# Kernel optimization log

Measured on AMD Instinct MI355X. Metric: run time of the kernel, lower is better.

## Reference

```python
import jax, jax.numpy as jnp
import numpy as np
from jax import lax

K = 3           # number of channel clusters (hard-coded in the torch forward)
KM_ITERS = 50   # fixed Lloyd iterations (stand-in for sklearn KMeans, random_state=0)

SEQ_LEN, PRED_LEN, CH, BATCH = 1024, 192, 1000, 32
LH = SEQ_LEN // 2


def _pairwise_sqdist(z, c):
    # z: [N, D], c: [K, D] -> [N, K]
    zz = jnp.sum(z * z, axis=1, keepdims=True)          # [N,1]
    cc = jnp.sum(c * c, axis=1)[None, :]                # [1,K]
    return zz - 2.0 * (z @ c.T) + cc


def kmeans_labels(z, k=K, iters=KM_ITERS):
    # Deterministic Lloyd's algorithm; init = first k rows (deterministic stand-in
    # for sklearn's k-means++ with random_state=0).
    c0 = z[:k]

    def step(c, _):
        d = _pairwise_sqdist(z, c)
        labels = jnp.argmin(d, axis=1)
        ones = jnp.ones((z.shape[0],), z.dtype)
        sums = jax.ops.segment_sum(z, labels, num_segments=k)       # [K,D]
        counts = jax.ops.segment_sum(ones, labels, num_segments=k)  # [K]
        new_c = jnp.where(counts[:, None] > 0,
                          sums / jnp.maximum(counts, 1.0)[:, None], c)
        return new_c, None

    c, _ = lax.scan(step, c0, None, length=iters)
    return jnp.argmin(_pairwise_sqdist(z, c), axis=1)   # [N] int32


def setup_inputs() -> dict:
    key = jax.random.key(0)
    ks = jax.random.split(key, 4)
    x = jax.random.normal(ks[0], (BATCH, SEQ_LEN, CH), dtype=jnp.float32)
    # stacked per-cluster expert Linears g1/g2/g3: weight [K, P, Lh], bias [K, P]
    Wg = jax.random.normal(ks[1], (K, PRED_LEN, LH), dtype=jnp.float32) * 0.02
    bg = jnp.zeros((K, PRED_LEN), dtype=jnp.float32)
    Wu = jax.random.normal(ks[2], (PRED_LEN, LH), dtype=jnp.float32) * 0.02
    bu = jnp.zeros((PRED_LEN,), dtype=jnp.float32)
    z1 = jnp.zeros((1,), dtype=jnp.float32)
    return {"x": x, "x_mark_enc": z1, "x_dec": z1, "x_mark_dec": z1,
            "Wg": Wg, "bg": bg, "Wu": Wu, "bu": bu}


def reference(x, x_mark_enc, x_dec, x_mark_dec, Wg, bg, Wu, bu):
    # instance normalization over time (torch.var is unbiased -> ddof=1)
    x_mean = jnp.mean(x, axis=1, keepdims=True)
    xc = x - x_mean
    x_var = jnp.var(xc, axis=1, keepdims=True, ddof=1) + 1e-5
    xn = xc / jnp.sqrt(x_var)

    # Haar split along time
    x1 = xn[:, 0::2, :] * 0.5
    x2 = xn[:, 1::2, :] * 0.5
    x_L = x1 + x2          # [B, Lh, N]
    x_U = x1 - x2          # [B, Lh, N]

    # channel clustering on z = x_L reshaped to [N, B*Lh]
    B, Lh, N = x_L.shape
    z = x_L.reshape(B * Lh, N).T                      # [N, B*Lh]
    labels = kmeans_labels(z)                         # [N]

    # per-cluster Linear experts expressed as per-channel gathered weights
    # (identical math to gather g_k -> g_kLinear -> scatter back)
    Wn = Wg[labels]                                   # [N, P, Lh]
    bn = bg[labels]                                   # [N, P]
    g = jnp.einsum('bln,npl->bpn', x_L, Wn) + bn.T[None]   # [B, P, N]

    xu = jnp.einsum('bln,pl->bpn', x_U, Wu) + bu[None, :, None]

    xy = xu + g
    return xy * jnp.sqrt(x_var) + x_mean
```

## Files before the change

kernel.cpp:

```cpp
#include <hip/hip_runtime.h>
#include <hip/hip_bf16.h>
#include <hip/hip_cooperative_groups.h>

namespace cg = cooperative_groups;

#define B_   32
#define L_   1024
#define LH_  512
#define CH_  1000
#define PRED_ 192
#define ITERS_ 50
#define KBL_ 16384
#define SLOTS_ 1012
#define NTILES_ 253
#define NT2_ 506
#define NTRI_ 36
#define SEG_ 16

typedef __attribute__((ext_vector_type(8))) _Float16 f16x8;
typedef __attribute__((ext_vector_type(4))) float f32x4;

__device__ inline ushort f2h(float x) {
    union { _Float16 h; ushort u; } c;
    c.h = (_Float16)x;
    return c.u;
}

__global__ __launch_bounds__(256) void k1_partial(const float* __restrict__ x,
                                                  float* __restrict__ pS,
                                                  float* __restrict__ pSS) {
    int seg = blockIdx.x;
    int b = blockIdx.y;
    int t = threadIdx.x;
    if (t >= 250) return;
    int c4 = t * 4;
    const float* xp = x + (size_t)b * L_ * CH_ + (size_t)seg * 64 * CH_ + c4;
    float4 s = {0.f, 0.f, 0.f, 0.f}, ss = {0.f, 0.f, 0.f, 0.f};
#pragma unroll 4
    for (int l = 0; l < 64; ++l) {
        float4 v = *(const float4*)(xp + (size_t)l * CH_);
        s.x += v.x; s.y += v.y; s.z += v.z; s.w += v.w;
        ss.x += v.x * v.x; ss.y += v.y * v.y; ss.z += v.z * v.z; ss.w += v.w * v.w;
    }
    size_t o = ((size_t)seg * B_ + b) * CH_ + c4;
    *(float4*)(pS + o) = s;
    *(float4*)(pSS + o) = ss;
}

__global__ __launch_bounds__(256) void k1b_reduce(const float* __restrict__ pS,
                                                  const float* __restrict__ pSS,
                                                  float* __restrict__ meanT,
                                                  float* __restrict__ sstdT,
                                                  float* __restrict__ invT) {
    int idx = blockIdx.x * 256 + threadIdx.x;
    if (idx >= B_ * CH_) return;
    int c = idx % CH_;
    int b = idx / CH_;
    float s = 0.f, ss = 0.f;
#pragma unroll
    for (int seg = 0; seg < SEG_; ++seg) {
        size_t o = ((size_t)seg * B_ + b) * CH_ + c;
        s += pS[o];
        ss += pSS[o];
    }
    float m = s * (1.0f / L_);
    float var = (ss - (float)L_ * m * m) * (1.0f / (L_ - 1)) + 1e-5f;
    float sd = sqrtf(var);
    meanT[c * B_ + b] = m;
    sstdT[c * B_ + b] = sd;
    invT[c * B_ + b] = 1.0f / sd;
}

__global__ __launch_bounds__(256) void k2_build(const float* __restrict__ x,
                                                const float* __restrict__ meanT,
                                                const float* __restrict__ invT,
                                                ushort* __restrict__ zLF,
                                                ushort* __restrict__ zUF) {
    __shared__ float Ls[32][33];
    __shared__ float Us[32][33];
    int tid = threadIdx.x;
    int tx = tid & 31, ty = tid >> 5;
    int n0 = blockIdx.x * 32;
    int lh0 = blockIdx.y * 32;
    int b = blockIdx.z;
    int n = n0 + tx;
    float m = 0.f, iv = 0.f;
    if (n < CH_) { m = meanT[n * B_ + b]; iv = invT[n * B_ + b]; }
    for (int r = 0; r < 4; ++r) {
        int lh = lh0 + ty + 8 * r;
        float v0 = 0.f, v1 = 0.f;
        if (n < CH_) {
            v0 = x[((size_t)b * L_ + 2 * lh) * CH_ + n];
            v1 = x[((size_t)b * L_ + 2 * lh + 1) * CH_ + n];
        }
        float a = (v0 - m) * iv * 0.5f;
        float c2 = (v1 - m) * iv * 0.5f;
        Ls[ty + 8 * r][tx] = a + c2;
        Us[ty + 8 * r][tx] = a - c2;
    }
    __syncthreads();
    for (int r = 0; r < 4; ++r) {
        int nl = ty + 8 * r;
        int nn = n0 + nl;
        if (nn < CH_) {
            size_t dst = (size_t)nn * KBL_ + (size_t)b * LH_ + lh0 + tx;
            zLF[dst] = f2h(Ls[tx][nl]);
            zUF[dst] = f2h(Us[tx][nl]);
        }
    }
}

__global__ __launch_bounds__(256) void k0_wprep(const float* __restrict__ Wg,
                                                const float* __restrict__ Wu,
                                                ushort* __restrict__ WF2) {
    int r = blockIdx.x;
    int p = r % PRED_;
    int tid = threadIdx.x;
#pragma unroll
    for (int i = 0; i < 4; ++i) {
        int k = i * 256 + tid;
        float w = (k < 512) ? Wg[(size_t)r * LH_ + k]
                            : Wu[(size_t)p * LH_ + (k - 512)];
        WF2[(size_t)r * 1024 + k] = f2h(w);
    }
}

#define ZSPLIT_ 16
#define KSEG_   1024
#define NT_     (KSEG_ / 32)

__global__ __launch_bounds__(256) void k3_mfma(const ushort* __restrict__ zF,
                                               float* __restrict__ gpart) {
    __shared__ __align__(16) ushort AH[128][40];
    __shared__ __align__(16) ushort BH[128][40];

    int bid = blockIdx.x;
    int xcd = bid & 7, w = bid >> 3;
    int ksl = 2 * xcd + (w >= NTRI_);
    int t = (w >= NTRI_) ? w - NTRI_ : w;
    int ti = 0, tt = t;
    while (tt >= 8 - ti) { tt -= 8 - ti; ++ti; }
    int tj = ti + tt;
    int i0 = ti * 128, j0 = tj * 128;
    int kb = ksl * KSEG_;

    int tid = threadIdx.x;
    int lane = tid & 63;
    int wid = tid >> 6;
    int wr = wid >> 1, wc = wid & 1;
    int fr = lane & 15;
    int g8 = lane >> 4;

    f32x4 acc[4][4];
#pragma unroll
    for (int m = 0; m < 4; ++m)
#pragma unroll
        for (int n = 0; n < 4; ++n) acc[m][n] = (f32x4){0.f, 0.f, 0.f, 0.f};

    int srow = tid >> 2;
    int sseg = tid & 3;

    uint4 pv[4];
    auto stage_load = [&](int kt) {
        int k0 = kb + kt * 32;
#pragma unroll
        for (int s = 0; s < 4; ++s) {
            int tile = s >> 1, rep = s & 1;
            int row = srow + rep * 64;
            int grow = ((tile == 0) ? i0 : j0) + row;
            uint4 v = {0u, 0u, 0u, 0u};
            if (grow < CH_)
                v = *(const uint4*)(zF + (size_t)grow * KBL_ + k0 + sseg * 8);
            pv[s] = v;
        }
    };
    auto stage_write = [&]() {
#pragma unroll
        for (int s = 0; s < 4; ++s) {
            int tile = s >> 1, rep = s & 1;
            int row = srow + rep * 64;
            ushort* dst = (tile == 0) ? &AH[row][sseg * 8] : &BH[row][sseg * 8];
            *(uint4*)dst = pv[s];
        }
    };

    stage_load(0);
    for (int t2 = 0; t2 < NT_; ++t2) {
        __syncthreads();
        stage_write();
        __syncthreads();
        if (t2 + 1 < NT_) stage_load(t2 + 1);

        f16x8 a[4];
#pragma unroll
        for (int m = 0; m < 4; ++m)
            a[m] = *(const f16x8*)&AH[wr * 64 + m * 16 + fr][g8 * 8];
#pragma unroll
        for (int n = 0; n < 4; ++n) {
            f16x8 bv = *(const f16x8*)&BH[wc * 64 + n * 16 + fr][g8 * 8];
#pragma unroll
            for (int m = 0; m < 4; ++m)
                acc[m][n] = __builtin_amdgcn_mfma_f32_16x16x32_f16(a[m], bv, acc[m][n], 0, 0, 0);
        }
    }

    float* gp = gpart + ((size_t)ksl * NTRI_ + t) * 16384;
#pragma unroll
    for (int m = 0; m < 4; ++m) {
        int rb = wr * 64 + m * 16 + g8 * 4;
#pragma unroll
        for (int n = 0; n < 4; ++n) {
            int c = wc * 64 + n * 16 + fr;
#pragma unroll
            for (int q = 0; q < 4; ++q)
                gp[(size_t)(rb + q) * 128 + c] = acc[m][n][q];
        }
    }
}

__global__ __launch_bounds__(256) void k3b_sym(const float* __restrict__ gpart,
                                               float* __restrict__ g) {
    int t = blockIdx.x;
    int seg = blockIdx.y;
    int ti = 0, tt = t;
    while (tt >= 8 - ti) { tt -= 8 - ti; ++ti; }
    int tj = ti + tt;
    int i0 = ti * 128, j0 = tj * 128;
    int tid = threadIdx.x;
    int e0 = seg * 4096 + tid * 16;
    int r = e0 >> 7, c0 = e0 & 127;

    float4 s[4];
#pragma unroll
    for (int j = 0; j < 4; ++j) s[j] = (float4){0.f, 0.f, 0.f, 0.f};
#pragma unroll
    for (int p = 0; p < ZSPLIT_; ++p) {
        const float* src = gpart + ((size_t)p * NTRI_ + t) * 16384 + e0;
#pragma unroll
        for (int j = 0; j < 4; ++j) {
            float4 v = *(const float4*)(src + j * 4);
            s[j].x += v.x; s[j].y += v.y; s[j].z += v.z; s[j].w += v.w;
        }
    }
    int i = i0 + r;
    if (i < CH_) {
#pragma unroll
        for (int j = 0; j < 4; ++j) {
            int jc = j0 + c0 + j * 4;
            if (jc + 3 < CH_) {
                *(float4*)(g + (size_t)i * CH_ + jc) = s[j];
            } else {
#pragma unroll
                for (int e = 0; e < 4; ++e)
                    if (jc + e < CH_) g[(size_t)i * CH_ + jc + e] = ((const float*)&s[j])[e];
            }
        }
        if (ti != tj) {
#pragma unroll
            for (int j = 0; j < 4; ++j) {
#pragma unroll
                for (int e = 0; e < 4; ++e) {
                    int jc = j0 + c0 + j * 4 + e;
                    if (jc < CH_) g[(size_t)jc * CH_ + i] = ((const float*)&s[j])[e];
                }
            }
        }
    }
}

__global__ __launch_bounds__(256) void k4a_init(const float* __restrict__ g,
                                                float* __restrict__ sbuf,
                                                float* __restrict__ ccG) {
    int i = blockIdx.x * 256 + threadIdx.x;
    if (i < CH_) {
        sbuf[i * 3 + 0] = g[(size_t)i * CH_ + 0];
        sbuf[i * 3 + 1] = g[(size_t)i * CH_ + 1];
        sbuf[i * 3 + 2] = g[(size_t)i * CH_ + 2];
    }
    if (i < 3) ccG[i] = g[(size_t)i * CH_ + i];
}

__global__ __launch_bounds__(1024) void k4_kmeans(const float* __restrict__ g,
                                                  float* __restrict__ sbuf,
                                                  float* __restrict__ ccG,
                                                  int* __restrict__ labels) {
    cg::grid_group grid = cg::this_grid();
    __shared__ int   lab[1024];
    __shared__ float red[3][1024];
    __shared__ int   cnt[4], cnt2[4], chgS;

    int tid = threadIdx.x;
    int bpt0 = blockIdx.x * 64;
    lab[tid] = (tid < 3) ? tid : 3;
    __syncthreads();

    int par = 0;
    for (int it = 1; it <= ITERS_ + 1; ++it) {
        const float* sp = sbuf + par * 3 * CH_;
        if (tid < 4) { cnt[tid] = 0; cnt2[tid] = 0; }
        if (tid == 0) chgS = 0;
        __syncthreads();
        float c0 = 0.f, c1 = 0.f, c2 = 0.f;
        int lbp = 3;
        if (tid < CH_) {
            lbp = lab[tid];
            atomicAdd(&cnt[lbp], 1);
            if (lbp < 3) {
                float sv = sp[tid * 3 + lbp];
                if (lbp == 0) c0 = sv; else if (lbp == 1) c1 = sv; else c2 = sv;
            }
        }
        red[0][tid] = c0; red[1][tid] = c1; red[2][tid] = c2;
        __syncthreads();
        for (int off = 512; off > 0; off >>= 1) {
            if (tid < off) {
                red[0][tid] += red[0][tid + off];
                red[1][tid] += red[1][tid + off];
                red[2][tid] += red[2][tid + off];
            }
            __syncthreads();
        }
        int n0 = cnt[0], n1 = cnt[1], n2 = cnt[2];
        float cc0 = (n0 > 0) ? red[0][0] / (float)n0 : ccG[par * 3 + 0];
        float cc1 = (n1 > 0) ? red[1][0] / (float)n1 : ccG[par * 3 + 1];
        float cc2 = (n2 > 0) ? red[2][0] / (float)n2 : ccG[par * 3 + 2];
        if (tid == 0) ccG[(par ^ 1) * 3 + 0] = cc0;
        if (tid == 1) ccG[(par ^ 1) * 3 + 1] = cc1;
        if (tid == 2) ccG[(par ^ 1) * 3 + 2] = cc2;

        int myNew = -1;
        if (tid < CH_) {
            float d0 = cc0 - 2.f * sp[tid * 3 + 0];
            float d1 = cc1 - 2.f * sp[tid * 3 + 1];
            float d2 = cc2 - 2.f * sp[tid * 3 + 2];
            int nl = 0; float dm = d0;
            if (d1 < dm) { dm = d1; nl = 1; }
            if (d2 < dm) { dm = d2; nl = 2; }
            if (nl != lbp) atomicAdd(&chgS, 1);
            myNew = nl;
        }
        __syncthreads();
        if (tid < CH_) { lab[tid] = myNew; atomicAdd(&cnt2[myNew], 1); }
        __syncthreads();

        if (it == ITERS_ + 1) break;
        if (chgS == 0 && it > 1) break;

        int n0n = cnt2[0], n1n = cnt2[1], n2n = cnt2[2];
        float* sq = sbuf + (par ^ 1) * 3 * CH_;
        int i = bpt0 + (tid >> 4);
        int sub = tid & 15;
        if (i < CH_) {
            const float* gr = g + (size_t)i * CH_;
            float a0 = 0.f, a1 = 0.f, a2 = 0.f;
            for (int j = sub; j < CH_; j += 16) {
                float gv = gr[j];
                int lb = lab[j];
                a0 += (lb == 0) ? gv : 0.f;
                a1 += (lb == 1) ? gv : 0.f;
                a2 += (lb == 2) ? gv : 0.f;
            }
#pragma unroll
            for (int msk = 1; msk < 16; msk <<= 1) {
                a0 += __shfl_xor(a0, msk, 16);
                a1 += __shfl_xor(a1, msk, 16);
                a2 += __shfl_xor(a2, msk, 16);
            }
            if (sub == 0) {
                sq[i * 3 + 0] = (n0n > 0) ? a0 / (float)n0n : sp[i * 3 + 0];
                sq[i * 3 + 1] = (n1n > 0) ? a1 / (float)n1n : sp[i * 3 + 1];
                sq[i * 3 + 2] = (n2n > 0) ? a2 / (float)n2n : sp[i * 3 + 2];
            }
        }
        par ^= 1;
        grid.sync();
    }

    if (tid < 64) {
        int i = bpt0 + tid;
        if (i < CH_) labels[i] = lab[i];
    }
}

__global__ __launch_bounds__(256) void k4b_perm(const int* __restrict__ labels,
                                                int* __restrict__ chlist,
                                                int* __restrict__ chpos,
                                                int* __restrict__ slabel) {
    __shared__ int cnt[3], st[4], c2[3];
    int tid = threadIdx.x;
    if (tid < 3) { cnt[tid] = 0; c2[tid] = 0; }
    __syncthreads();
    for (int n = tid; n < CH_; n += 256) atomicAdd(&cnt[labels[n]], 1);
    __syncthreads();
    if (tid == 0) {
        st[0] = 0;
        st[1] = ((cnt[0] + 3) >> 2) << 2;
        st[2] = st[1] + (((cnt[1] + 3) >> 2) << 2);
        st[3] = st[2] + (((cnt[2] + 3) >> 2) << 2);
    }
    __syncthreads();
    for (int s = tid; s < SLOTS_; s += 256) chlist[s] = 0;
    for (int t = tid; t < NTILES_; t += 256) {
        int s = t * 4;
        slabel[t] = (s < st[1]) ? 0 : (s < st[2]) ? 1 : (s < st[3]) ? 2 : 0;
    }
    __syncthreads();
    for (int n = tid; n < CH_; n += 256) {
        int lb = labels[n];
        int r = atomicAdd(&c2[lb], 1);
        int slot = st[lb] + r;
        chlist[slot] = n;
        chpos[n] = slot;
    }
}

__global__ __launch_bounds__(256) void k5_grouped(const ushort* __restrict__ zLF,
                                                  const ushort* __restrict__ zUF,
                                                  const ushort* __restrict__ WF2,
                                                  const int* __restrict__ chlist,
                                                  const int* __restrict__ slabel,
                                                  const float* __restrict__ bg,
                                                  const float* __restrict__ bu,
                                                  const float* __restrict__ meanT,
                                                  const float* __restrict__ sstdT,
                                                  float* __restrict__ outP) {
    __shared__ __align__(16) ushort ZT[64][40];
    __shared__ __align__(16) ushort WT[192][40];
    __shared__ int sch[2];

    int tile = blockIdx.x;
    int tid = threadIdx.x;
    if (tid < 2) sch[tid] = chlist[tile * 2 + tid];
    int lab = slabel[tile >> 1];
    __syncthreads();

    int lane = tid & 63, wid = tid >> 6;
    int fr = lane & 15, g8 = lane >> 4;

    int srow = tid >> 2, sseg = tid & 3;
    size_t zb = (size_t)sch[srow >> 5] * KBL_ + (size_t)(srow & 31) * LH_;
    const ushort* wbase = WF2 + (size_t)(lab * PRED_) * 1024;

    f32x4 acc[4][3];
#pragma unroll
    for (int m = 0; m < 4; ++m)
#pragma unroll
        for (int n = 0; n < 3; ++n) acc[m][n] = (f32x4){0.f, 0.f, 0.f, 0.f};

    uint4 pz, pw0, pw1, pw2;
    auto stage_load = [&](int t) {
        const ushort* zsrc = (t < 16) ? zLF : zUF;
        int ko = ((t & 15) * 32) + sseg * 8;
        pz  = *(const uint4*)(zsrc + zb + ko);
        int kw = t * 32 + sseg * 8;
        pw0 = *(const uint4*)(wbase + (size_t)srow * 1024 + kw);
        pw1 = *(const uint4*)(wbase + (size_t)(srow + 64) * 1024 + kw);
        pw2 = *(const uint4*)(wbase + (size_t)(srow + 128) * 1024 + kw);
    };
    auto stage_write = [&]() {
        *(uint4*)&ZT[srow][sseg * 8] = pz;
        *(uint4*)&WT[srow][sseg * 8] = pw0;
        *(uint4*)&WT[srow + 64][sseg * 8] = pw1;
        *(uint4*)&WT[srow + 128][sseg * 8] = pw2;
    };

    stage_load(0);
    for (int t = 0; t < 32; ++t) {
        __syncthreads();
        stage_write();
        __syncthreads();
        if (t + 1 < 32) stage_load(t + 1);

        f16x8 a[4];
#pragma unroll
        for (int m = 0; m < 4; ++m)
            a[m] = *(const f16x8*)&ZT[m * 16 + fr][g8 * 8];
#pragma unroll
        for (int nf = 0; nf < 3; ++nf) {
            f16x8 bv = *(const f16x8*)&WT[wid * 48 + nf * 16 + fr][g8 * 8];
#pragma unroll
            for (int m = 0; m < 4; ++m)
                acc[m][nf] = __builtin_amdgcn_mfma_f32_16x16x32_f16(a[m], bv, acc[m][nf], 0, 0, 0);
        }
    }

#pragma unroll
    for (int m = 0; m < 4; ++m) {
#pragma unroll
        for (int q = 0; q < 4; ++q) {
            int sb = m * 16 + g8 * 4 + q;
            int sl = sb >> 5, b = sb & 31;
            int n = sch[sl];
            float sd = sstdT[n * B_ + b], mu = meanT[n * B_ + b];
            size_t obase = ((size_t)(tile * 2 + sl) * B_ + b) * PRED_;
#pragma unroll
            for (int nf = 0; nf < 3; ++nf) {
                int p = wid * 48 + nf * 16 + fr;
                float v = acc[m][nf][q] + bg[lab * PRED_ + p] + bu[p];
                outP[obase + p] = v * sd + mu;
            }
        }
    }
}

__global__ __launch_bounds__(256) void k7_unperm(const float* __restrict__ outP,
                                                 const int* __restrict__ chpos,
                                                 float* __restrict__ out) {
    int n = blockIdx.x * 256 + threadIdx.x;
    int p0 = blockIdx.y * 32;
    int b = blockIdx.z;
    if (n >= CH_) return;
    const float* src = outP + ((size_t)chpos[n] * B_ + b) * PRED_ + p0;
    float4 v[8];
#pragma unroll
    for (int j = 0; j < 8; ++j) v[j] = *(const float4*)(src + j * 4);
#pragma unroll
    for (int j = 0; j < 8; ++j) {
#pragma unroll
        for (int e = 0; e < 4; ++e) {
            int p = p0 + j * 4 + e;
            out[((size_t)b * PRED_ + p) * CH_ + n] = ((const float*)&v[j])[e];
        }
    }
}

extern "C" void kernel_launch(void* const* d_in, const int* in_sizes, int n_in,
                              void* d_out, int out_size, void* d_ws, size_t ws_size,
                              hipStream_t stream) {
    const float* x  = (const float*)d_in[0];
    const float* Wg = (const float*)d_in[4];
    const float* bg = (const float*)d_in[5];
    const float* Wu = (const float*)d_in[6];
    const float* bu = (const float*)d_in[7];
    float* out = (float*)d_out;
    (void)in_sizes; (void)n_in; (void)out_size; (void)ws_size;

    char* ws = (char*)d_ws;
    size_t off = 0;
    auto alloc = [&](size_t bytes) {
        void* p = ws + off;
        off = (off + bytes + 255) & ~(size_t)255;
        return p;
    };
    ushort* zLF  = (ushort*)alloc((size_t)16384000 * 2);
    ushort* zUF  = (ushort*)alloc((size_t)16384000 * 2);
    float*  G    = (float*)alloc((size_t)1000000 * 4);
    ushort* WF2  = (ushort*)alloc((size_t)576 * 1024 * 2);
    float*  meanT = (float*)alloc((size_t)32000 * 4);
    float*  sstdT = (float*)alloc((size_t)32000 * 4);
    float*  invT  = (float*)alloc((size_t)32000 * 4);
    float*  pS   = (float*)alloc((size_t)SEG_ * B_ * CH_ * 4);
    float*  pSS  = (float*)alloc((size_t)SEG_ * B_ * CH_ * 4);
    int*    labels  = (int*)alloc((size_t)1024 * 4);
    float*  sbuf = (float*)alloc((size_t)2 * 3 * CH_ * 4);
    float*  ccG  = (float*)alloc((size_t)8 * 4);
    int*    chlist = (int*)alloc((size_t)SLOTS_ * 4);
    int*    chpos  = (int*)alloc((size_t)1024 * 4);
    int*    slabel = (int*)alloc((size_t)256 * 4);
    char* unionBase = (char*)alloc((size_t)ZSPLIT_ * NTRI_ * 16384 * 4);
    float* Gp   = (float*)unionBase;
    float* outP = (float*)unionBase;

    k1_partial<<<dim3(SEG_, 32), 256, 0, stream>>>(x, pS, pSS);
    k1b_reduce<<<125, 256, 0, stream>>>(pS, pSS, meanT, sstdT, invT);
    k2_build<<<dim3(32, 16, 32), 256, 0, stream>>>(x, meanT, invT, zLF, zUF);
    k0_wprep<<<576, 256, 0, stream>>>(Wg, Wu, WF2);
    k3_mfma<<<8 * NTRI_ * 2, 256, 0, stream>>>(zLF, Gp);
    k3b_sym<<<dim3(NTRI_, 4), 256, 0, stream>>>(Gp, G);
    k4a_init<<<4, 256, 0, stream>>>(G, sbuf, ccG);
    void* args[] = { (void*)&G, (void*)&sbuf, (void*)&ccG, (void*)&labels };
    hipLaunchCooperativeKernel((void*)k4_kmeans, dim3(16), dim3(1024), args, 0, stream);
    k4b_perm<<<1, 256, 0, stream>>>(labels, chlist, chpos, slabel);
    k5_grouped<<<NT2_, 256, 0, stream>>>(zLF, zUF, WF2, chlist, slabel,
                                         bg, bu, meanT, sstdT, outP);
    k7_unperm<<<dim3(4, 6, 32), 256, 0, stream>>>(outP, chpos, out);
}
```

Before: 223.3 us.

## Fold kmeans init and permutation into cooperative kernel, use wave reductions

Removes the separate init and permutation kernels by reading initial centroid scores straight from the Gram matrix on the first iteration and building the cluster permutation in block 0 after the loop. Replaces the 10-step shared-memory tree reduction and per-thread atomics with wave shuffle reductions and ballot/popcount counts, which cuts the __syncthreads barriers in each of up to 50 iterations. Centroid norms and counts are carried in shared memory across iterations instead of being reloaded from global. This saves two launches and per-iteration sync latency, at the cost of more complex state handling.

Result: faster. 214.2 us (-4.1%).

```diff
diff --git a/kernel.cpp b/kernel.cpp
--- a/kernel.cpp
+++ b/kernel.cpp
@@ -268,79 +268,91 @@
     }
 }
 
-__global__ __launch_bounds__(256) void k4a_init(const float* __restrict__ g,
-                                                float* __restrict__ sbuf,
-                                                float* __restrict__ ccG) {
-    int i = blockIdx.x * 256 + threadIdx.x;
-    if (i < CH_) {
-        sbuf[i * 3 + 0] = g[(size_t)i * CH_ + 0];
-        sbuf[i * 3 + 1] = g[(size_t)i * CH_ + 1];
-        sbuf[i * 3 + 2] = g[(size_t)i * CH_ + 2];
-    }
-    if (i < 3) ccG[i] = g[(size_t)i * CH_ + i];
-}
-
 __global__ __launch_bounds__(1024) void k4_kmeans(const float* __restrict__ g,
                                                   float* __restrict__ sbuf,
-                                                  float* __restrict__ ccG,
-                                                  int* __restrict__ labels) {
+                                                  int* __restrict__ chlist,
+                                                  int* __restrict__ chpos,
+                                                  int* __restrict__ slabel) {
     cg::grid_group grid = cg::this_grid();
     __shared__ int   lab[1024];
-    __shared__ float red[3][1024];
-    __shared__ int   cnt[4], cnt2[4], chgS;
+    __shared__ float wred[16][3];
+    __shared__ float ccS[3];
+    __shared__ float ccPrev[3];
+    __shared__ int   cntPrev[3];
+    __shared__ int   cnt2[3];
+    __shared__ int   chgS;
+    __shared__ int   st[4], c2r[3];
 
     int tid = threadIdx.x;
+    int wv = tid >> 6, ln = tid & 63;
     int bpt0 = blockIdx.x * 64;
-    lab[tid] = (tid < 3) ? tid : 3;
+
+    int lbp = (tid < 3) ? tid : 3;
+    lab[tid] = lbp;
+    if (tid < 3) {
+        cntPrev[tid] = 1;
+        ccPrev[tid] = g[(size_t)tid * CH_ + tid];
+    }
     __syncthreads();
 
     int par = 0;
     for (int it = 1; it <= ITERS_ + 1; ++it) {
         const float* sp = sbuf + par * 3 * CH_;
-        if (tid < 4) { cnt[tid] = 0; cnt2[tid] = 0; }
-        if (tid == 0) chgS = 0;
-        __syncthreads();
-        float c0 = 0.f, c1 = 0.f, c2 = 0.f;
-        int lbp = 3;
+        float s0 = 0.f, s1 = 0.f, s2 = 0.f;
         if (tid < CH_) {
-            lbp = lab[tid];
-            atomicAdd(&cnt[lbp], 1);
-            if (lbp < 3) {
-                float sv = sp[tid * 3 + lbp];
-                if (lbp == 0) c0 = sv; else if (lbp == 1) c1 = sv; else c2 = sv;
-            }
-        }
-        red[0][tid] = c0; red[1][tid] = c1; red[2][tid] = c2;
-        __syncthreads();
-        for (int off = 512; off > 0; off >>= 1) {
-            if (tid < off) {
-                red[0][tid] += red[0][tid + off];
-                red[1][tid] += red[1][tid + off];
-                red[2][tid] += red[2][tid + off];
-            }
-            __syncthreads();
-        }
-        int n0 = cnt[0], n1 = cnt[1], n2 = cnt[2];
-        float cc0 = (n0 > 0) ? red[0][0] / (float)n0 : ccG[par * 3 + 0];
-        float cc1 = (n1 > 0) ? red[1][0] / (float)n1 : ccG[par * 3 + 1];
-        float cc2 = (n2 > 0) ? red[2][0] / (float)n2 : ccG[par * 3 + 2];
-        if (tid == 0) ccG[(par ^ 1) * 3 + 0] = cc0;
-        if (tid == 1) ccG[(par ^ 1) * 3 + 1] = cc1;
-        if (tid == 2) ccG[(par ^ 1) * 3 + 2] = cc2;
-
-        int myNew = -1;
+            if (it == 1) {
+                const float* gr = g + (size_t)tid * CH_;
+                s0 = gr[0]; s1 = gr[1]; s2 = gr[2];
+            } else {
+                s0 = sp[tid * 3 + 0]; s1 = sp[tid * 3 + 1]; s2 = sp[tid * 3 + 2];
+            }
+        }
+        float c0 = (lbp == 0) ? s0 : 0.f;
+        float c1 = (lbp == 1) ? s1 : 0.f;
+        float c2 = (lbp == 2) ? s2 : 0.f;
+#pragma unroll
+        for (int m = 1; m < 64; m <<= 1) {
+            c0 += __shfl_xor(c0, m);
+            c1 += __shfl_xor(c1, m);
+            c2 += __shfl_xor(c2, m);
+        }
+        if (ln == 0) { wred[wv][0] = c0; wred[wv][1] = c1; wred[wv][2] = c2; }
+        if (tid == 0) { cnt2[0] = 0; cnt2[1] = 0; cnt2[2] = 0; chgS = 0; }
+        __syncthreads();
+        if (tid < 3) {
+            float sacc = 0.f;
+#pragma unroll
+            for (int w2 = 0; w2 < 16; ++w2) sacc += wred[w2][tid];
+            int n = cntPrev[tid];
+            float cc = (n > 0) ? sacc / (float)n : ccPrev[tid];
+            ccS[tid] = cc;
+            ccPrev[tid] = cc;
+        }
+        __syncthreads();
+        float cc0 = ccS[0], cc1 = ccS[1], cc2 = ccS[2];
+
+        int nl = lbp;
         if (tid < CH_) {
-            float d0 = cc0 - 2.f * sp[tid * 3 + 0];
-            float d1 = cc1 - 2.f * sp[tid * 3 + 1];
-            float d2 = cc2 - 2.f * sp[tid * 3 + 2];
-            int nl = 0; float dm = d0;
+            float d0 = cc0 - 2.f * s0;
+            float d1 = cc1 - 2.f * s1;
+            float d2 = cc2 - 2.f * s2;
+            nl = 0; float dm = d0;
             if (d1 < dm) { dm = d1; nl = 1; }
             if (d2 < dm) { dm = d2; nl = 2; }
-            if (nl != lbp) atomicAdd(&chgS, 1);
-            myNew = nl;
-        }
-        __syncthreads();
-        if (tid < CH_) { lab[tid] = myNew; atomicAdd(&cnt2[myNew], 1); }
+        }
+        bool act = (tid < CH_);
+        unsigned long long b0 = __ballot(act && nl == 0);
+        unsigned long long b1 = __ballot(act && nl == 1);
+        unsigned long long b2 = __ballot(act && nl == 2);
+        unsigned long long bc = __ballot(act && nl != lbp);
+        if (ln == 0) {
+            if (b0) atomicAdd(&cnt2[0], (int)__popcll(b0));
+            if (b1) atomicAdd(&cnt2[1], (int)__popcll(b1));
+            if (b2) atomicAdd(&cnt2[2], (int)__popcll(b2));
+            if (bc) atomicAdd(&chgS, (int)__popcll(bc));
+        }
+        lab[tid] = nl;
+        lbp = nl;
         __syncthreads();
 
         if (it == ITERS_ + 1) break;
@@ -367,50 +379,41 @@
                 a2 += __shfl_xor(a2, msk, 16);
             }
             if (sub == 0) {
-                sq[i * 3 + 0] = (n0n > 0) ? a0 / (float)n0n : sp[i * 3 + 0];
-                sq[i * 3 + 1] = (n1n > 0) ? a1 / (float)n1n : sp[i * 3 + 1];
-                sq[i * 3 + 2] = (n2n > 0) ? a2 / (float)n2n : sp[i * 3 + 2];
-            }
-        }
+                float f0, f1, f2;
+                if (it == 1) { f0 = gr[0]; f1 = gr[1]; f2 = gr[2]; }
+                else { f0 = sp[i * 3 + 0]; f1 = sp[i * 3 + 1]; f2 = sp[i * 3 + 2]; }
+                sq[i * 3 + 0] = (n0n > 0) ? a0 / (float)n0n : f0;
+                sq[i * 3 + 1] = (n1n > 0) ? a1 / (float)n1n : f1;
+                sq[i * 3 + 2] = (n2n > 0) ? a2 / (float)n2n : f2;
+            }
+        }
+        if (tid < 3) cntPrev[tid] = cnt2[tid];
         par ^= 1;
         grid.sync();
     }
 
-    if (tid < 64) {
-        int i = bpt0 + tid;
-        if (i < CH_) labels[i] = lab[i];
-    }
-}
-
-__global__ __launch_bounds__(256) void k4b_perm(const int* __restrict__ labels,
-                                                int* __restrict__ chlist,
-                                                int* __restrict__ chpos,
-                                                int* __restrict__ slabel) {
-    __shared__ int cnt[3], st[4], c2[3];
-    int tid = threadIdx.x;
-    if (tid < 3) { cnt[tid] = 0; c2[tid] = 0; }
-    __syncthreads();
-    for (int n = tid; n < CH_; n += 256) atomicAdd(&cnt[labels[n]], 1);
-    __syncthreads();
-    if (tid == 0) {
-        st[0] = 0;
-        st[1] = ((cnt[0] + 3) >> 2) << 2;
-        st[2] = st[1] + (((cnt[1] + 3) >> 2) << 2);
-        st[3] = st[2] + (((cnt[2] + 3) >> 2) << 2);
-    }
-    __syncthreads();
-    for (int s = tid; s < SLOTS_; s += 256) chlist[s] = 0;
-    for (int t = tid; t < NTILES_; t += 256) {
-        int s = t * 4;
-        slabel[t] = (s < st[1]) ? 0 : (s < st[2]) ? 1 : (s < st[3]) ? 2 : 0;
-    }
-    __syncthreads();
-    for (int n = tid; n < CH_; n += 256) {
-        int lb = labels[n];
-        int r = atomicAdd(&c2[lb], 1);
-        int slot = st[lb] + r;
-        chlist[slot] = n;
-        chpos[n] = slot;
+    if (blockIdx.x == 0) {
+        if (tid == 0) {
+            st[0] = 0;
+            st[1] = ((cnt2[0] + 3) >> 2) << 2;
+            st[2] = st[1] + (((cnt2[1] + 3) >> 2) << 2);
+            st[3] = st[2] + (((cnt2[2] + 3) >> 2) << 2);
+            c2r[0] = 0; c2r[1] = 0; c2r[2] = 0;
+        }
+        __syncthreads();
+        if (tid < SLOTS_) chlist[tid] = 0;
+        if (tid < NTILES_) {
+            int s = tid * 4;
+            slabel[tid] = (s < st[1]) ? 0 : (s < st[2]) ? 1 : (s < st[3]) ? 2 : 0;
+        }
+        __syncthreads();
+        if (tid < CH_) {
+            int lb = lab[tid];
+            int r = atomicAdd(&c2r[lb], 1);
+            int slot = st[lb] + r;
+            chlist[slot] = tid;
+            chpos[tid] = slot;
+        }
     }
 }
 
@@ -551,9 +554,7 @@
     float*  invT  = (float*)alloc((size_t)32000 * 4);
     float*  pS   = (float*)alloc((size_t)SEG_ * B_ * CH_ * 4);
     float*  pSS  = (float*)alloc((size_t)SEG_ * B_ * CH_ * 4);
-    int*    labels  = (int*)alloc((size_t)1024 * 4);
     float*  sbuf = (float*)alloc((size_t)2 * 3 * CH_ * 4);
-    float*  ccG  = (float*)alloc((size_t)8 * 4);
     int*    chlist = (int*)alloc((size_t)SLOTS_ * 4);
     int*    chpos  = (int*)alloc((size_t)1024 * 4);
     int*    slabel = (int*)alloc((size_t)256 * 4);
@@ -567,10 +568,8 @@
     k0_wprep<<<576, 256, 0, stream>>>(Wg, Wu, WF2);
     k3_mfma<<<8 * NTRI_ * 2, 256, 0, stream>>>(zLF, Gp);
     k3b_sym<<<dim3(NTRI_, 4), 256, 0, stream>>>(Gp, G);
-    k4a_init<<<4, 256, 0, stream>>>(G, sbuf, ccG);
-    void* args[] = { (void*)&G, (void*)&sbuf, (void*)&ccG, (void*)&labels };
+    void* args[] = { (void*)&G, (void*)&sbuf, (void*)&chlist, (void*)&chpos, (void*)&slabel };
     hipLaunchCooperativeKernel((void*)k4_kmeans, dim3(16), dim3(1024), args, 0, stream);
-    k4b_perm<<<1, 256, 0, stream>>>(labels, chlist, chpos, slabel);
     k5_grouped<<<NT2_, 256, 0, stream>>>(zLF, zUF, WF2, chlist, slabel,
                                          bg, bu, meanT, sstdT, outP);
     k7_unperm<<<dim3(4, 6, 32), 256, 0, stream>>>(outP, chpos, out);
```
